# Kernel tuning notes

Hardware: AMD Instinct MI355X
Metric: run time of the kernel (lower is better)

Reference implementation:

```python
import jax, jax.numpy as jnp
import numpy as np

B, N, D, V, Y = 4, 4096, 512, 50257, 16000

def setup_inputs() -> dict:
    key = jax.random.key(0)
    ks = jax.random.split(key, 5)
    # token ids in [1, V): avoid pad_id=0 so no attention row is fully -inf
    M_s = jax.random.randint(ks[0], (B, N), 1, V)
    E_v = jax.random.normal(ks[1], (V, D), jnp.float32) * 0.02
    E_y = jax.random.normal(ks[2], (Y, D), jnp.float32) * 0.02
    s = 1.0 / np.sqrt(D)  # kaiming_uniform(a=sqrt(5)) bound for [D,D]
    W_A = jax.random.uniform(ks[3], (D, D), jnp.float32, minval=-s, maxval=s)
    W_O = jax.random.uniform(ks[4], (D, D), jnp.float32, minval=-s, maxval=s)
    gamma = jnp.ones((D,), jnp.float32)
    beta = jnp.zeros((D,), jnp.float32)
    return {"M_s": M_s, "E_v": E_v, "E_y": E_y, "W_A": W_A, "W_O": W_O,
            "gamma": gamma, "beta": beta}

def _layer_norm(x, g, b, eps=1e-5):
    mu = jnp.mean(x, axis=-1, keepdims=True)
    var = jnp.mean(jnp.square(x - mu), axis=-1, keepdims=True)
    return (x - mu) * jax.lax.rsqrt(var + eps) * g + b

def reference(M_s, E_v, E_y, W_A, W_O, gamma, beta):
    # Self-attention branch (v_q=None), dropout in eval mode (identity).
    X = E_v[M_s]                                   # [B, N, D]
    mask = (M_s != 0)                              # [B, N] padding mask
    # logits = (X @ W_A) @ X^T
    logits = jnp.einsum('bnd,de,bme->bnm', X, W_A, X)   # [B, N, N]
    logits = jnp.where(mask[:, None, :], logits, -jnp.inf)
    # positional + causal bias: D = -|i-j| with future (i<j) set to -inf
    i = jnp.arange(N, dtype=jnp.float32)[:, None]
    j = jnp.arange(N, dtype=jnp.float32)[None, :]
    dist = i - j
    bias = jnp.where(dist >= 0, -dist, -jnp.inf)        # [N, N]
    A = jax.nn.softmax(logits + bias, axis=-1)          # [B, N, N]
    Q_c = jnp.einsum('bnm,bmd,de->bne', A, X, W_O)      # [B, N, D]
    H = _layer_norm(Q_c + X, gamma, beta)               # [B, N, D]
    y_logits = jnp.einsum('bnd,yd->bny', H, E_y)        # [B, N, Y]
    return y_logits, A
```

## Files before the change

### kernel.cpp

```cpp
#include <hip/hip_runtime.h>


#define DEVINL __device__ __forceinline__

typedef __attribute__((ext_vector_type(8))) short bf16x8;
typedef __attribute__((ext_vector_type(4))) float f32x4;
typedef unsigned short u16;

#define BB 4
#define NN 4096
#define DD 512
#define YY 16000
#define ROWS (BB * NN)

DEVINL u16 f2bf(float x) {
  unsigned u = __float_as_uint(x);
  return (u16)((u + 0x7fffu + ((u >> 16) & 1u)) >> 16);
}

DEVINL void gload16(const void* g, void* l) {
  __builtin_amdgcn_global_load_lds(
      (const __attribute__((address_space(1))) void*)g,
      (__attribute__((address_space(3))) void*)l, 16, 0, 0);
}

DEVINL void zero_acc(f32x4 acc[4][4]) {
#pragma unroll
  for (int m = 0; m < 4; ++m)
#pragma unroll
    for (int n = 0; n < 4; ++n) {
      acc[m][n][0] = 0.f; acc[m][n][1] = 0.f;
      acc[m][n][2] = 0.f; acc[m][n][3] = 0.f;
    }
}

DEVINL void gemm_bt_core(const u16* __restrict__ A, int lda,
                         const u16* __restrict__ Bm, int ldb, int ksteps,
                         u16* sA, u16* sB, f32x4 acc[4][4], int tid) {
  const int lane = tid & 63, w = tid >> 6;
  const int wr = (w >> 1) * 64, wc = (w & 1) * 64;
  const int c0 = w * 128 + lane, c1 = c0 + 64;
  const u16* gA0 = A + (size_t)(c0 >> 2) * lda + (c0 & 3) * 8;
  const u16* gA1 = A + (size_t)(c1 >> 2) * lda + (c1 & 3) * 8;
  const u16* gB0 = Bm + (size_t)(c0 >> 2) * ldb + (c0 & 3) * 8;
  const u16* gB1 = Bm + (size_t)(c1 >> 2) * ldb + (c1 & 3) * 8;
  u16* lA0 = sA + w * 1024;  u16* lA1 = lA0 + 512;
  u16* lB0 = sB + w * 1024;  u16* lB1 = lB0 + 512;
  const int fr = lane & 15, fk = (lane >> 4) * 8;

  for (int kt = 0; kt < ksteps; ++kt) {
    __syncthreads();
    gload16(gA0 + kt * 32, lA0);
    gload16(gA1 + kt * 32, lA1);
    gload16(gB0 + kt * 32, lB0);
    gload16(gB1 + kt * 32, lB1);
    __syncthreads();
    bf16x8 af[4], bfv[4];
#pragma unroll
    for (int m = 0; m < 4; ++m)
      af[m] = *(const bf16x8*)(sA + (wr + m * 16 + fr) * 32 + fk);
#pragma unroll
    for (int n = 0; n < 4; ++n)
      bfv[n] = *(const bf16x8*)(sB + (wc + n * 16 + fr) * 32 + fk);
#pragma unroll
    for (int m = 0; m < 4; ++m)
#pragma unroll
      for (int n = 0; n < 4; ++n)
        acc[m][n] = __builtin_amdgcn_mfma_f32_16x16x32_bf16(af[m], bfv[n],
                                                            acc[m][n], 0, 0, 0);
  }
}

DEVINL void gemm_a32_core(const float* __restrict__ A, int lda,
                          const u16* __restrict__ Bm, int ldb, int ksteps,
                          u16* sA, u16* sB, f32x4 acc[4][4], int tid) {
  const int lane = tid & 63, w = tid >> 6;
  const int wr = (w >> 1) * 64, wc = (w & 1) * 64;
  const int c0 = w * 128 + lane, c1 = c0 + 64;
  const u16* gB0 = Bm + (size_t)(c0 >> 2) * ldb + (c0 & 3) * 8;
  const u16* gB1 = Bm + (size_t)(c1 >> 2) * ldb + (c1 & 3) * 8;
  u16* lB0 = sB + w * 1024;  u16* lB1 = lB0 + 512;
  const int fr = lane & 15, fk = (lane >> 4) * 8;
  const int acol = (tid & 7) * 4;
  const int arow0 = tid >> 3;

  for (int kt = 0; kt < ksteps; ++kt) {
    __syncthreads();
    gload16(gB0 + kt * 32, lB0);
    gload16(gB1 + kt * 32, lB1);
#pragma unroll
    for (int p = 0; p < 4; ++p) {
      int row = arow0 + 32 * p;
      float4 v = *(const float4*)(A + (size_t)row * lda + kt * 32 + acol);
      ushort4 hv = make_ushort4(f2bf(v.x), f2bf(v.y), f2bf(v.z), f2bf(v.w));
      *(ushort4*)(sA + row * 32 + acol) = hv;
    }
    __syncthreads();
    bf16x8 af[4], bfv[4];
#pragma unroll
    for (int m = 0; m < 4; ++m)
      af[m] = *(const bf16x8*)(sA + (wr + m * 16 + fr) * 32 + fk);
#pragma unroll
    for (int n = 0; n < 4; ++n)
      bfv[n] = *(const bf16x8*)(sB + (wc + n * 16 + fr) * 32 + fk);
#pragma unroll
    for (int m = 0; m < 4; ++m)
#pragma unroll
      for (int n = 0; n < 4; ++n)
        acc[m][n] = __builtin_amdgcn_mfma_f32_16x16x32_bf16(af[m], bfv[n],
                                                            acc[m][n], 0, 0, 0);
  }
}

__global__ __launch_bounds__(128) void prep_gather(const int* __restrict__ Ms,
                                                   const float* __restrict__ Ev,
                                                   u16* __restrict__ Xb) {
  int row = blockIdx.x, tid = threadIdx.x;
  int tok = Ms[row];
  float4 v = *(const float4*)(Ev + (size_t)tok * DD + tid * 4);
  *(ushort4*)(Xb + (size_t)row * DD + tid * 4) =
      make_ushort4(f2bf(v.x), f2bf(v.y), f2bf(v.z), f2bf(v.w));
}

__global__ __launch_bounds__(256) void prep_wt(const float* __restrict__ W,
                                               u16* __restrict__ Wt) {
  int idx = blockIdx.x * 256 + threadIdx.x;
  int d = idx >> 9, e = idx & 511;
  Wt[(size_t)e * DD + d] = f2bf(W[idx]);
}

__global__ __launch_bounds__(256) void prep_ey(const float* __restrict__ Ey,
                                               u16* __restrict__ Eyb) {
  size_t i4 = (size_t)blockIdx.x * 256 + threadIdx.x;
  float4 v = *(const float4*)(Ey + i4 * 4);
  *(ushort4*)(Eyb + i4 * 4) =
      make_ushort4(f2bf(v.x), f2bf(v.y), f2bf(v.z), f2bf(v.w));
}

__global__ __launch_bounds__(256) void prep_xt(const u16* __restrict__ Xb,
                                               u16* __restrict__ XbT) {
  __shared__ u16 t[64][65];
  int tid = threadIdx.x;
  int nt = blockIdx.x, dt = blockIdx.y, b = blockIdx.z;
  const u16* src = Xb + ((size_t)b * NN + nt * 64) * DD + dt * 64;
#pragma unroll
  for (int p = 0; p < 16; ++p) {
    int e = tid + 256 * p; int r = e >> 6, c = e & 63;
    t[r][c] = src[(size_t)r * DD + c];
  }
  __syncthreads();
  u16* dst = XbT + ((size_t)b * DD + dt * 64) * NN + nt * 64;
#pragma unroll
  for (int p = 0; p < 16; ++p) {
    int e = tid + 256 * p; int r = e >> 6, c = e & 63;
    dst[(size_t)r * NN + c] = t[c][r];
  }
}

__global__ __launch_bounds__(256) void k2_xw(const u16* __restrict__ Xb,
                                             const u16* __restrict__ WAt,
                                             u16* __restrict__ XWb) {
  __shared__ u16 sA[4096], sB[4096];
  f32x4 acc[4][4]; zero_acc(acc);
  int tid = threadIdx.x;
  size_t row0 = (size_t)blockIdx.x * 128, col0 = (size_t)blockIdx.y * 128;
  gemm_bt_core(Xb + row0 * DD, DD, WAt + col0 * DD, DD, DD / 32, sA, sB, acc, tid);
  int lane = tid & 63, w = tid >> 6;
  int wr = (w >> 1) * 64, wc = (w & 1) * 64;
  int cr = (lane >> 4) * 4, cc = lane & 15;
#pragma unroll
  for (int m = 0; m < 4; ++m)
#pragma unroll
    for (int n = 0; n < 4; ++n)
#pragma unroll
      for (int r = 0; r < 4; ++r) {
        size_t gi = row0 + wr + m * 16 + cr + r;
        size_t gj = col0 + wc + n * 16 + cc;
        XWb[gi * DD + gj] = f2bf(acc[m][n][r]);
      }
}

__global__ __launch_bounds__(256) void k3_scores(const u16* __restrict__ XWb,
                                                 const u16* __restrict__ Xb,
                                                 const int* __restrict__ Ms,
                                                 float* __restrict__ Aout) {
  int ib = blockIdx.x, jb = blockIdx.y, b = blockIdx.z;
  if (jb > ib) return;
  __shared__ u16 sA[4096], sB[4096];
  f32x4 acc[4][4]; zero_acc(acc);
  int tid = threadIdx.x;
  const u16* Ap = XWb + ((size_t)b * NN + ib * 128) * DD;
  const u16* Bp = Xb  + ((size_t)b * NN + jb * 128) * DD;
  gemm_bt_core(Ap, DD, Bp, DD, DD / 32, sA, sB, acc, tid);
  int lane = tid & 63, w = tid >> 6;
  int wr = (w >> 1) * 64, wc = (w & 1) * 64;
  int cr = (lane >> 4) * 4, cc = lane & 15;
  float* Ab = Aout + (size_t)b * NN * NN;
#pragma unroll
  for (int m = 0; m < 4; ++m)
#pragma unroll
    for (int n = 0; n < 4; ++n)
#pragma unroll
      for (int r = 0; r < 4; ++r) {
        int i = ib * 128 + wr + m * 16 + cr + r;
        int j = jb * 128 + wc + n * 16 + cc;
        float v = acc[m][n][r] - (float)(i - j);
        if (j > i) v = -1e30f;
        if (Ms[b * NN + j] == 0) v = -1e30f;
        Ab[(size_t)i * NN + j] = v;
      }
}

__global__ __launch_bounds__(256) void k4_softmax(float* __restrict__ Aout) {
  __shared__ float srow[NN];
  __shared__ float red[4];
  size_t row = blockIdx.x;
  int i = (int)(row & (NN - 1));
  float* S = Aout + row * (size_t)NN;
  int len = i + 1, tid = threadIdx.x;
  int nv = len >> 2;
  for (int v = tid; v < nv; v += 256)
    *(float4*)(srow + v * 4) = *(const float4*)(S + v * 4);
  for (int k = (nv << 2) + tid; k < len; k += 256) srow[k] = S[k];
  __syncthreads();
  float m = -3.0e38f;
  for (int k = tid; k < len; k += 256) m = fmaxf(m, srow[k]);
#pragma unroll
  for (int o = 32; o; o >>= 1) m = fmaxf(m, __shfl_xor(m, o));
  if ((tid & 63) == 0) red[tid >> 6] = m;
  __syncthreads();
  m = fmaxf(fmaxf(red[0], red[1]), fmaxf(red[2], red[3]));
  float l = 0.f;
  for (int k = tid; k < len; k += 256) {
    float e = expf(srow[k] - m);
    srow[k] = e; l += e;
  }
  __syncthreads();
#pragma unroll
  for (int o = 32; o; o >>= 1) l += __shfl_xor(l, o);
  if ((tid & 63) == 0) red[tid >> 6] = l;
  __syncthreads();
  float inv = 1.f / (red[0] + red[1] + red[2] + red[3]);
  for (int k = tid; k < NN; k += 256)
    S[k] = (k < len) ? srow[k] * inv : 0.f;
}

__global__ __launch_bounds__(256) void k5_ax(const float* __restrict__ Aout,
                                             const u16* __restrict__ XbT,
                                             u16* __restrict__ AXb) {
  int ib = blockIdx.x, db = blockIdx.y, b = blockIdx.z;
  __shared__ u16 sA[4096], sB[4096];
  f32x4 acc[4][4]; zero_acc(acc);
  int tid = threadIdx.x;
  const float* Ap = Aout + ((size_t)b * NN + ib * 128) * NN;
  const u16*   Bp = XbT + ((size_t)b * DD + db * 128) * NN;
  int ksteps = (ib + 1) * 4;
  gemm_a32_core(Ap, NN, Bp, NN, ksteps, sA, sB, acc, tid);
  int lane = tid & 63, w = tid >> 6;
  int wr = (w >> 1) * 64, wc = (w & 1) * 64;
  int cr = (lane >> 4) * 4, cc = lane & 15;
#pragma unroll
  for (int m = 0; m < 4; ++m)
#pragma unroll
    for (int n = 0; n < 4; ++n)
#pragma unroll
      for (int r = 0; r < 4; ++r) {
        int i = ib * 128 + wr + m * 16 + cr + r;
        int d = db * 128 + wc + n * 16 + cc;
        AXb[((size_t)b * NN + i) * DD + d] = f2bf(acc[m][n][r]);
      }
}

__global__ __launch_bounds__(256) void k6_qc(const u16* __restrict__ AXb,
                                             const u16* __restrict__ WOt,
                                             float* __restrict__ Qc32) {
  __shared__ u16 sA[4096], sB[4096];
  f32x4 acc[4][4]; zero_acc(acc);
  int tid = threadIdx.x;
  size_t row0 = (size_t)blockIdx.x * 128, col0 = (size_t)blockIdx.y * 128;
  gemm_bt_core(AXb + row0 * DD, DD, WOt + col0 * DD, DD, DD / 32, sA, sB, acc, tid);
  int lane = tid & 63, w = tid >> 6;
  int wr = (w >> 1) * 64, wc = (w & 1) * 64;
  int cr = (lane >> 4) * 4, cc = lane & 15;
#pragma unroll
  for (int m = 0; m < 4; ++m)
#pragma unroll
    for (int n = 0; n < 4; ++n)
#pragma unroll
      for (int r = 0; r < 4; ++r) {
        size_t gi = row0 + wr + m * 16 + cr + r;
        size_t gj = col0 + wc + n * 16 + cc;
        Qc32[gi * DD + gj] = acc[m][n][r];
      }
}

__global__ __launch_bounds__(128) void k6b_ln(const float* __restrict__ Qc,
                                              const float* __restrict__ Ev,
                                              const int* __restrict__ Ms,
                                              const float* __restrict__ gamma,
                                              const float* __restrict__ beta,
                                              u16* __restrict__ Hb) {
  int row = blockIdx.x, tid = threadIdx.x;
  int tok = Ms[row];
  float4 q = *(const float4*)(Qc + (size_t)row * DD + tid * 4);
  float4 x = *(const float4*)(Ev + (size_t)tok * DD + tid * 4);
  float v0 = q.x + x.x, v1 = q.y + x.y, v2 = q.z + x.z, v3 = q.w + x.w;
  float s = v0 + v1 + v2 + v3;
  float s2 = v0 * v0 + v1 * v1 + v2 * v2 + v3 * v3;
#pragma unroll
  for (int o = 32; o; o >>= 1) { s += __shfl_xor(s, o); s2 += __shfl_xor(s2, o); }
  __shared__ float r1[2], r2[2];
  int lane = tid & 63, w = tid >> 6;
  if (lane == 0) { r1[w] = s; r2[w] = s2; }
  __syncthreads();
  s = r1[0] + r1[1]; s2 = r2[0] + r2[1];
  float mu = s * (1.f / 512.f);
  float var = s2 * (1.f / 512.f) - mu * mu;
  float rs = 1.f / sqrtf(var + 1e-5f);
  float4 g  = *(const float4*)(gamma + tid * 4);
  float4 be = *(const float4*)(beta + tid * 4);
  ushort4 h = make_ushort4(f2bf((v0 - mu) * rs * g.x + be.x),
                           f2bf((v1 - mu) * rs * g.y + be.y),
                           f2bf((v2 - mu) * rs * g.z + be.z),
                           f2bf((v3 - mu) * rs * g.w + be.w));
  *(ushort4*)(Hb + (size_t)row * DD + tid * 4) = h;
}

__global__ __launch_bounds__(256) void k7_logits(const u16* __restrict__ Hb,
                                                 const u16* __restrict__ Eyb,
                                                 float* __restrict__ Yout) {
  __shared__ u16 sA[4096], sB[4096];
  f32x4 acc[4][4]; zero_acc(acc);
  int tid = threadIdx.x;
  size_t row0 = (size_t)blockIdx.x * 128, col0 = (size_t)blockIdx.y * 128;
  gemm_bt_core(Hb + row0 * DD, DD, Eyb + col0 * DD, DD, DD / 32, sA, sB, acc, tid);
  int lane = tid & 63, w = tid >> 6;
  int wr = (w >> 1) * 64, wc = (w & 1) * 64;
  int cr = (lane >> 4) * 4, cc = lane & 15;
#pragma unroll
  for (int m = 0; m < 4; ++m)
#pragma unroll
    for (int n = 0; n < 4; ++n)
#pragma unroll
      for (int r = 0; r < 4; ++r) {
        size_t gi = row0 + wr + m * 16 + cr + r;
        size_t gj = col0 + wc + n * 16 + cc;
        Yout[gi * YY + gj] = acc[m][n][r];
      }
}

extern "C" void kernel_launch(void* const* d_in, const int* in_sizes, int n_in,
                              void* d_out, int out_size, void* d_ws, size_t ws_size,
                              hipStream_t stream) {
  (void)in_sizes; (void)n_in; (void)out_size; (void)ws_size;
  const int*   Ms    = (const int*)d_in[0];
  const float* Ev    = (const float*)d_in[1];
  const float* Ey    = (const float*)d_in[2];
  const float* WA    = (const float*)d_in[3];
  const float* WO    = (const float*)d_in[4];
  const float* gamma = (const float*)d_in[5];
  const float* beta  = (const float*)d_in[6];

  float* Yout = (float*)d_out;
  float* Aout = Yout + (size_t)BB * NN * YY;

  char* w = (char*)d_ws;
  u16* Xb  = (u16*)w; w += (size_t)ROWS * DD * 2;
  u16* XbT = (u16*)w; w += (size_t)BB * DD * NN * 2;
  u16* XWb = (u16*)w; w += (size_t)ROWS * DD * 2;
  u16* AXb = (u16*)w; w += (size_t)ROWS * DD * 2;
  u16* Hb  = (u16*)w; w += (size_t)ROWS * DD * 2;
  u16* WAt = (u16*)w; w += (size_t)DD * DD * 2;
  u16* WOt = (u16*)w; w += (size_t)DD * DD * 2;
  u16* Eyb = (u16*)w; w += (size_t)YY * DD * 2;
  float* Qc32 = (float*)XbT;

  prep_gather<<<ROWS, 128, 0, stream>>>(Ms, Ev, Xb);
  prep_wt<<<1024, 256, 0, stream>>>(WA, WAt);
  prep_wt<<<1024, 256, 0, stream>>>(WO, WOt);
  prep_ey<<<8000, 256, 0, stream>>>(Ey, Eyb);
  prep_xt<<<dim3(NN / 64, DD / 64, BB), 256, 0, stream>>>(Xb, XbT);
  k2_xw<<<dim3(ROWS / 128, DD / 128), 256, 0, stream>>>(Xb, WAt, XWb);
  k3_scores<<<dim3(NN / 128, NN / 128, BB), 256, 0, stream>>>(XWb, Xb, Ms, Aout);
  k4_softmax<<<ROWS, 256, 0, stream>>>(Aout);
  k5_ax<<<dim3(NN / 128, DD / 128, BB), 256, 0, stream>>>(Aout, XbT, AXb);
  k6_qc<<<dim3(ROWS / 128, DD / 128), 256, 0, stream>>>(AXb, WOt, Qc32);
  k6b_ln<<<ROWS, 128, 0, stream>>>(Qc32, Ev, Ms, gamma, beta, Hb);
  k7_logits<<<dim3(ROWS / 128, YY / 128), 256, 0, stream>>>(Hb, Eyb, Yout);
}
```

Baseline: 1.005 ms.

## Retile logits GEMM with 256x256 double-buffered tiles and feed AX from bf16 softmax copy

The output-logits GEMM becomes a 512-thread kernel with 256x256 tiles, swizzled LDS loads via global_load_lds, double buffering over K, setprio around MFMA bursts, and a swizzled block order for L2 reuse. E_y is padded to 16128 rows so the tiles divide evenly, and the stores are guarded. The softmax now also writes a bf16 copy of the attention matrix, padded to 128 columns, so the A@X GEMM can use the pure-bf16 loader instead of converting fp32 in the loop. The cost is extra bf16 writes and 128MB of additional workspace.

```diff
diff --git a/kernel.cpp b/kernel.cpp
--- a/kernel.cpp
+++ b/kernel.cpp
@@ -11,6 +11,7 @@
 #define NN 4096
 #define DD 512
 #define YY 16000
+#define YPAD 16128
 #define ROWS (BB * NN)
 
 DEVINL u16 f2bf(float x) {
@@ -71,47 +72,6 @@
   }
 }
 
-DEVINL void gemm_a32_core(const float* __restrict__ A, int lda,
-                          const u16* __restrict__ Bm, int ldb, int ksteps,
-                          u16* sA, u16* sB, f32x4 acc[4][4], int tid) {
-  const int lane = tid & 63, w = tid >> 6;
-  const int wr = (w >> 1) * 64, wc = (w & 1) * 64;
-  const int c0 = w * 128 + lane, c1 = c0 + 64;
-  const u16* gB0 = Bm + (size_t)(c0 >> 2) * ldb + (c0 & 3) * 8;
-  const u16* gB1 = Bm + (size_t)(c1 >> 2) * ldb + (c1 & 3) * 8;
-  u16* lB0 = sB + w * 1024;  u16* lB1 = lB0 + 512;
-  const int fr = lane & 15, fk = (lane >> 4) * 8;
-  const int acol = (tid & 7) * 4;
-  const int arow0 = tid >> 3;
-
-  for (int kt = 0; kt < ksteps; ++kt) {
-    __syncthreads();
-    gload16(gB0 + kt * 32, lB0);
-    gload16(gB1 + kt * 32, lB1);
-#pragma unroll
-    for (int p = 0; p < 4; ++p) {
-      int row = arow0 + 32 * p;
-      float4 v = *(const float4*)(A + (size_t)row * lda + kt * 32 + acol);
-      ushort4 hv = make_ushort4(f2bf(v.x), f2bf(v.y), f2bf(v.z), f2bf(v.w));
-      *(ushort4*)(sA + row * 32 + acol) = hv;
-    }
-    __syncthreads();
-    bf16x8 af[4], bfv[4];
-#pragma unroll
-    for (int m = 0; m < 4; ++m)
-      af[m] = *(const bf16x8*)(sA + (wr + m * 16 + fr) * 32 + fk);
-#pragma unroll
-    for (int n = 0; n < 4; ++n)
-      bfv[n] = *(const bf16x8*)(sB + (wc + n * 16 + fr) * 32 + fk);
-#pragma unroll
-    for (int m = 0; m < 4; ++m)
-#pragma unroll
-      for (int n = 0; n < 4; ++n)
-        acc[m][n] = __builtin_amdgcn_mfma_f32_16x16x32_bf16(af[m], bfv[n],
-                                                            acc[m][n], 0, 0, 0);
-  }
-}
-
 __global__ __launch_bounds__(128) void prep_gather(const int* __restrict__ Ms,
                                                    const float* __restrict__ Ev,
                                                    u16* __restrict__ Xb) {
@@ -132,9 +92,15 @@
 __global__ __launch_bounds__(256) void prep_ey(const float* __restrict__ Ey,
                                                u16* __restrict__ Eyb) {
   size_t i4 = (size_t)blockIdx.x * 256 + threadIdx.x;
-  float4 v = *(const float4*)(Ey + i4 * 4);
-  *(ushort4*)(Eyb + i4 * 4) =
-      make_ushort4(f2bf(v.x), f2bf(v.y), f2bf(v.z), f2bf(v.w));
+  size_t row = i4 >> 7;
+  ushort4 h;
+  if (row < YY) {
+    float4 v = *(const float4*)(Ey + i4 * 4);
+    h = make_ushort4(f2bf(v.x), f2bf(v.y), f2bf(v.z), f2bf(v.w));
+  } else {
+    h = make_ushort4(0, 0, 0, 0);
+  }
+  *(ushort4*)(Eyb + i4 * 4) = h;
 }
 
 __global__ __launch_bounds__(256) void prep_xt(const u16* __restrict__ Xb,
@@ -211,7 +177,8 @@
       }
 }
 
-__global__ __launch_bounds__(256) void k4_softmax(float* __restrict__ Aout) {
+__global__ __launch_bounds__(256) void k4_softmax(float* __restrict__ Aout,
+                                                  u16* __restrict__ Abf) {
   __shared__ float srow[NN];
   __shared__ float red[4];
   size_t row = blockIdx.x;
@@ -241,21 +208,25 @@
   if ((tid & 63) == 0) red[tid >> 6] = l;
   __syncthreads();
   float inv = 1.f / (red[0] + red[1] + red[2] + red[3]);
-  for (int k = tid; k < NN; k += 256)
-    S[k] = (k < len) ? srow[k] * inv : 0.f;
-}
-
-__global__ __launch_bounds__(256) void k5_ax(const float* __restrict__ Aout,
+  int padend = (len + 127) & ~127;
+  u16* Ab16 = Abf + row * (size_t)NN;
+  for (int k = tid; k < NN; k += 256) {
+    float a = (k < len) ? srow[k] * inv : 0.f;
+    S[k] = a;
+    if (k < padend) Ab16[k] = f2bf(a);
+  }
+}
+
+__global__ __launch_bounds__(256) void k5_ax(const u16* __restrict__ Abf,
                                              const u16* __restrict__ XbT,
                                              u16* __restrict__ AXb) {
   int ib = blockIdx.x, db = blockIdx.y, b = blockIdx.z;
   __shared__ u16 sA[4096], sB[4096];
   f32x4 acc[4][4]; zero_acc(acc);
   int tid = threadIdx.x;
-  const float* Ap = Aout + ((size_t)b * NN + ib * 128) * NN;
-  const u16*   Bp = XbT + ((size_t)b * DD + db * 128) * NN;
-  int ksteps = (ib + 1) * 4;
-  gemm_a32_core(Ap, NN, Bp, NN, ksteps, sA, sB, acc, tid);
+  const u16* Ap = Abf + ((size_t)b * NN + ib * 128) * NN;
+  const u16* Bp = XbT + ((size_t)b * DD + db * 128) * NN;
+  gemm_bt_core(Ap, NN, Bp, NN, (ib + 1) * 4, sA, sB, acc, tid);
   int lane = tid & 63, w = tid >> 6;
   int wr = (w >> 1) * 64, wc = (w & 1) * 64;
   int cr = (lane >> 4) * 4, cc = lane & 15;
@@ -326,27 +297,155 @@
   *(ushort4*)(Hb + (size_t)row * DD + tid * 4) = h;
 }
 
-__global__ __launch_bounds__(256) void k7_logits(const u16* __restrict__ Hb,
-                                                 const u16* __restrict__ Eyb,
-                                                 float* __restrict__ Yout) {
-  __shared__ u16 sA[4096], sB[4096];
-  f32x4 acc[4][4]; zero_acc(acc);
-  int tid = threadIdx.x;
-  size_t row0 = (size_t)blockIdx.x * 128, col0 = (size_t)blockIdx.y * 128;
-  gemm_bt_core(Hb + row0 * DD, DD, Eyb + col0 * DD, DD, DD / 32, sA, sB, acc, tid);
-  int lane = tid & 63, w = tid >> 6;
-  int wr = (w >> 1) * 64, wc = (w & 1) * 64;
-  int cr = (lane >> 4) * 4, cc = lane & 15;
-#pragma unroll
-  for (int m = 0; m < 4; ++m)
-#pragma unroll
-    for (int n = 0; n < 4; ++n)
-#pragma unroll
-      for (int r = 0; r < 4; ++r) {
-        size_t gi = row0 + wr + m * 16 + cr + r;
-        size_t gj = col0 + wc + n * 16 + cc;
-        Yout[gi * YY + gj] = acc[m][n][r];
+#define K7_STAGE(kt, buf)                                      \
+  {                                                            \
+    const u16* a0 = Ag + (kt) * 64;                            \
+    const u16* b0 = Bg + (kt) * 64;                            \
+    u16* Lb = lds + (buf) * 32768;                             \
+    gload16(a0 + offE0, Lb + d0);                              \
+    gload16(a0 + offE1, Lb + d1);                              \
+    gload16(a0 + 65536 + offE0, Lb + 8192 + d0);               \
+    gload16(a0 + 65536 + offE1, Lb + 8192 + d1);               \
+    gload16(b0 + offE0, Lb + 16384 + d0);                      \
+    gload16(b0 + offE1, Lb + 16384 + d1);                      \
+    gload16(b0 + 65536 + offE0, Lb + 24576 + d0);              \
+    gload16(b0 + 65536 + offE1, Lb + 24576 + d1);              \
+  }
+
+__global__ __launch_bounds__(512, 2) void k7_logits(const u16* __restrict__ Hb,
+                                                    const u16* __restrict__ Eyb,
+                                                    float* __restrict__ Yout) {
+  __shared__ u16 lds[65536];
+  const int tid = threadIdx.x;
+  const int lane = tid & 63, w = tid >> 6;
+  const int wm = w >> 2, wn = w & 3;
+
+  int id = blockIdx.x;
+  int swz = (id & 7) * (4032 / 8) + (id >> 3);
+  size_t row0 = (size_t)(swz & 63) * 256;
+  size_t col0 = (size_t)(swz >> 6) * 256;
+  const u16* Ag = Hb + row0 * DD;
+  const u16* Bg = Eyb + col0 * DD;
+
+  int offE0, offE1;
+  {
+    int q = tid;
+    int r = (((q >> 6) >> 1) << 4) | ((q >> 2) & 15);
+    int c = (((q >> 6) & 1) << 5) |
+            (((q & 3) << 3) ^ (((q >> 5) & 1) << 4) ^ (((q >> 4) & 1) << 3));
+    offE0 = r * DD + c;
+    q = 512 + tid;
+    r = (((q >> 6) >> 1) << 4) | ((q >> 2) & 15);
+    c = (((q >> 6) & 1) << 5) |
+        (((q & 3) << 3) ^ (((q >> 5) & 1) << 4) ^ (((q >> 4) & 1) << 3));
+    offE1 = r * DD + c;
+  }
+  const int d0 = w * 512, d1 = 4096 + w * 512;
+
+  int x = (lane & 15) * 64 + ((lane >> 4) & 3) * 16;
+  int fxu = (x ^ (((x >> 9) & 1) << 5) ^ (((x >> 8) & 1) << 4)) >> 1;
+
+  f32x4 acc[8][4];
+#pragma unroll
+  for (int m = 0; m < 8; ++m)
+#pragma unroll
+    for (int n = 0; n < 4; ++n) {
+      acc[m][n][0] = 0.f; acc[m][n][1] = 0.f;
+      acc[m][n][2] = 0.f; acc[m][n][3] = 0.f;
+    }
+
+  K7_STAGE(0, 0);
+  K7_STAGE(1, 1);
+  asm volatile("s_waitcnt vmcnt(8)" ::: "memory");
+  __syncthreads();
+
+  for (int c = 0; c < 8; ++c) {
+    const u16* L = lds + (c & 1) * 32768;
+    const u16* pa = L + wm * 8192;
+    const u16* pb = L + 16384 + (wn >> 1) * 8192 + (wn & 1) * 4096;
+    bf16x8 af[4][2], bf[4][2];
+#pragma unroll
+    for (int n = 0; n < 2; ++n)
+#pragma unroll
+      for (int ks = 0; ks < 2; ++ks)
+        bf[n][ks] = *(const bf16x8*)(pb + (n * 2 + ks) * 512 + fxu);
+#pragma unroll
+    for (int m = 0; m < 4; ++m)
+#pragma unroll
+      for (int ks = 0; ks < 2; ++ks)
+        af[m][ks] = *(const bf16x8*)(pa + (m * 2 + ks) * 512 + fxu);
+    __builtin_amdgcn_s_setprio(1);
+#pragma unroll
+    for (int m = 0; m < 4; ++m)
+#pragma unroll
+      for (int n = 0; n < 2; ++n)
+#pragma unroll
+        for (int ks = 0; ks < 2; ++ks)
+          acc[m][n] = __builtin_amdgcn_mfma_f32_16x16x32_bf16(
+              af[m][ks], bf[n][ks], acc[m][n], 0, 0, 0);
+    __builtin_amdgcn_s_setprio(0);
+#pragma unroll
+    for (int n = 2; n < 4; ++n)
+#pragma unroll
+      for (int ks = 0; ks < 2; ++ks)
+        bf[n][ks] = *(const bf16x8*)(pb + (n * 2 + ks) * 512 + fxu);
+    __builtin_amdgcn_s_setprio(1);
+#pragma unroll
+    for (int m = 0; m < 4; ++m)
+#pragma unroll
+      for (int n = 2; n < 4; ++n)
+#pragma unroll
+        for (int ks = 0; ks < 2; ++ks)
+          acc[m][n] = __builtin_amdgcn_mfma_f32_16x16x32_bf16(
+              af[m][ks], bf[n][ks], acc[m][n], 0, 0, 0);
+    __builtin_amdgcn_s_setprio(0);
+#pragma unroll
+    for (int m = 0; m < 4; ++m)
+#pragma unroll
+      for (int ks = 0; ks < 2; ++ks)
+        af[m][ks] = *(const bf16x8*)(pa + ((m + 4) * 2 + ks) * 512 + fxu);
+    __builtin_amdgcn_s_setprio(1);
+#pragma unroll
+    for (int m = 0; m < 4; ++m)
+#pragma unroll
+      for (int n = 0; n < 2; ++n)
+#pragma unroll
+        for (int ks = 0; ks < 2; ++ks)
+          acc[m + 4][n] = __builtin_amdgcn_mfma_f32_16x16x32_bf16(
+              af[m][ks], bf[n][ks], acc[m + 4][n], 0, 0, 0);
+#pragma unroll
+    for (int m = 0; m < 4; ++m)
+#pragma unroll
+      for (int n = 2; n < 4; ++n)
+#pragma unroll
+        for (int ks = 0; ks < 2; ++ks)
+          acc[m + 4][n] = __builtin_amdgcn_mfma_f32_16x16x32_bf16(
+              af[m][ks], bf[n][ks], acc[m + 4][n], 0, 0, 0);
+    __builtin_amdgcn_s_setprio(0);
+
+    __syncthreads();
+    if (c < 6) {
+      K7_STAGE(c + 2, c & 1);
+      asm volatile("s_waitcnt vmcnt(8)" ::: "memory");
+    } else if (c == 6) {
+      asm volatile("s_waitcnt vmcnt(0)" ::: "memory");
+    }
+    __syncthreads();
+  }
+
+  const int cr = (lane >> 4) * 4, cc = lane & 15;
+#pragma unroll
+  for (int m = 0; m < 8; ++m)
+#pragma unroll
+    for (int n = 0; n < 4; ++n) {
+      size_t gj = col0 + wn * 64 + n * 16 + cc;
+      if (gj < YY) {
+        size_t gi = row0 + wm * 128 + m * 16 + cr;
+#pragma unroll
+        for (int rr = 0; rr < 4; ++rr)
+          Yout[(gi + rr) * (size_t)YY + gj] = acc[m][n][rr];
       }
+    }
 }
 
 extern "C" void kernel_launch(void* const* d_in, const int* in_sizes, int n_in,
@@ -372,19 +471,20 @@
   u16* Hb  = (u16*)w; w += (size_t)ROWS * DD * 2;
   u16* WAt = (u16*)w; w += (size_t)DD * DD * 2;
   u16* WOt = (u16*)w; w += (size_t)DD * DD * 2;
-  u16* Eyb = (u16*)w; w += (size_t)YY * DD * 2;
+  u16* Eyb = (u16*)w; w += (size_t)YPAD * DD * 2;
+  u16* Abf = (u16*)w; w += (size_t)ROWS * NN * 2;
   float* Qc32 = (float*)XbT;
 
   prep_gather<<<ROWS, 128, 0, stream>>>(Ms, Ev, Xb);
   prep_wt<<<1024, 256, 0, stream>>>(WA, WAt);
   prep_wt<<<1024, 256, 0, stream>>>(WO, WOt);
-  prep_ey<<<8000, 256, 0, stream>>>(Ey, Eyb);
+  prep_ey<<<YPAD * DD / 4 / 256, 256, 0, stream>>>(Ey, Eyb);
   prep_xt<<<dim3(NN / 64, DD / 64, BB), 256, 0, stream>>>(Xb, XbT);
   k2_xw<<<dim3(ROWS / 128, DD / 128), 256, 0, stream>>>(Xb, WAt, XWb);
   k3_scores<<<dim3(NN / 128, NN / 128, BB), 256, 0, stream>>>(XWb, Xb, Ms, Aout);
-  k4_softmax<<<ROWS, 256, 0, stream>>>(Aout);
-  k5_ax<<<dim3(NN / 128, DD / 128, BB), 256, 0, stream>>>(Aout, XbT, AXb);
+  k4_softmax<<<ROWS, 256, 0, stream>>>(Aout, Abf);
+  k5_ax<<<dim3(NN / 128, DD / 128, BB), 256, 0, stream>>>(Abf, XbT, AXb);
   k6_qc<<<dim3(ROWS / 128, DD / 128), 256, 0, stream>>>(AXb, WOt, Qc32);
   k6b_ln<<<ROWS, 128, 0, stream>>>(Qc32, Ev, Ms, gamma, beta, Hb);
-  k7_logits<<<dim3(ROWS / 128, YY / 128), 256, 0, stream>>>(Hb, Eyb, Yout);
-}
+  k7_logits<<<dim3(64 * 63), 512, 0, stream>>>(Hb, Eyb, Yout);
+}
```

Measured after the change: 936.4 us (median of 4 runs). -6.8%, faster.
